# Kernel tuning notes

Hardware: AMD Instinct MI355X
Metric: run time of the kernel (lower is better)

## Reference

```python
import jax, jax.numpy as jnp
import numpy as np

B, S, D_IN, D_OUT, DEPTH = 4, 2048, 2048, 2048, 11
N_NODES = 2 ** (DEPTH + 1) - 1  # 4095


def setup_inputs() -> dict:
    key = jax.random.key(0)
    k1, k2, k3 = jax.random.split(key, 3)
    x = jax.random.normal(k1, (B, S, D_IN), dtype=jnp.float32)
    # scale weights like Linear init (~1/sqrt(fan_in)) to keep logits sane
    w_in = jax.random.normal(k2, (N_NODES, D_IN), dtype=jnp.float32) * (1.0 / np.sqrt(D_IN))
    w_out = jax.random.normal(k3, (D_OUT, N_NODES), dtype=jnp.float32) * (1.0 / np.sqrt(N_NODES))
    return {"x": x, "w_in": w_in, "w_out": w_out}


def reference(x, w_in, w_out):
    # x: [B,S,D_in]; w_in: [n_nodes, D_in]; w_out: [D_out, n_nodes]
    b, s, _ = x.shape
    cur = jnp.zeros((b, s), dtype=jnp.int32)
    nodes, logits = [], []
    for _ in range(DEPTH + 1):  # fixed, small depth loop (12 iters)
        nodes.append(cur)
        coeffs = w_in[cur]                       # [B,S,D_in] data-dependent gather
        score = jnp.einsum('bsd,bsd->bs', x, coeffs)  # per-token dot product
        logits.append(score)
        cur = cur * 2 + (score >= 0).astype(jnp.int32) + 1
    all_nodes = jnp.stack(nodes, axis=-1)        # [B,S,depth+1]
    all_logits = jnp.stack(logits, axis=-1)      # [B,S,depth+1]
    sel = w_out.T[all_nodes]                     # [B,S,depth+1,D_out]
    mlp1 = jax.nn.gelu(all_logits, approximate=False)  # torch nn.GELU default = exact erf
    return jnp.einsum('bsl,bslw->bsw', mlp1, sel)      # [B,S,D_out]
```

## Files before the change

### kernel.cpp

```cpp
#include <hip/hip_runtime.h>


#define D_IN    2048
#define D_OUT   2048
#define DEPTHP1 12
#define N_NODES 4095
#define N_TOK   8192
#define N_LEAF  2048

typedef float f4 __attribute__((ext_vector_type(4)));

__global__ __launch_bounds__(256) void transpose_wout64z(
    const float* __restrict__ in, float* __restrict__ out,
    int* __restrict__ hc ) {
    __shared__ float tile[64][65];
    const int fb = blockIdx.y * 64 + blockIdx.x;
    const int tx = threadIdx.x;
    const int ty = threadIdx.y;
    if (fb < 16) {
        const int i = fb * 256 + ty * 64 + tx;
        hc[i] = 0;
    }
    const int n0 = blockIdx.x * 64;
    const int j0 = blockIdx.y * 64;
    const int n = n0 + tx;
#pragma unroll
    for (int k = 0; k < 16; k++) {
        const int r = ty * 16 + k;
        if (n < N_NODES) tile[r][tx] = in[(size_t)(j0 + r) * N_NODES + n];
    }
    __syncthreads();
#pragma unroll
    for (int k = 0; k < 16; k++) {
        const int r = ty * 16 + k;
        const int nn = n0 + r;
        if (nn < N_NODES) out[(size_t)nn * D_OUT + (j0 + tx)] = tile[tx][r];
    }
}

__global__ __launch_bounds__(256) void phaseA(
    const float* __restrict__ x,
    const float* __restrict__ w_in,
    float* __restrict__ g_all,
    int* __restrict__ leaf,
    int* __restrict__ hist) {
    extern __shared__ float xs[];
    const int wave  = threadIdx.x >> 6;
    const int lane  = threadIdx.x & 63;
    const int token = blockIdx.x * 4 + wave;

    float4* xw = (float4*)(xs) + wave * (D_IN / 4);
    const float4* xrow = (const float4*)(x + (size_t)token * D_IN);
#pragma unroll
    for (int c = 0; c < 8; c++) xw[lane + 64 * c] = xrow[lane + 64 * c];

    int cur = 0;
#pragma unroll
    for (int l = 0; l < DEPTHP1; l++) {
        const float4* wrow = (const float4*)(w_in + (size_t)cur * D_IN);
        float p0 = 0.f, p1 = 0.f, p2 = 0.f, p3 = 0.f;
#pragma unroll
        for (int c = 0; c < 8; c++) {
            const float4 wc = wrow[lane + 64 * c];
            const float4 xc = xw[lane + 64 * c];
            float* p = (c < 2) ? &p0 : (c < 4) ? &p1 : (c < 6) ? &p2 : &p3;
            *p += wc.x * xc.x + wc.y * xc.y + wc.z * xc.z + wc.w * xc.w;
        }
        float part = (p0 + p1) + (p2 + p3);
#pragma unroll
        for (int off = 32; off >= 1; off >>= 1)
            part += __shfl_xor(part, off, 64);
        const float score = part;
        cur = 2 * cur + 1 + (score >= 0.f ? 1 : 0);
        const float g = 0.5f * score * (1.0f + erff(score * 0.70710678118654752f));
        if (lane == 0) g_all[token * DEPTHP1 + l] = g;
    }
    if (lane == 0) {
        const int leafid = ((cur - 1) >> 1) - (N_LEAF - 1);
        leaf[token] = leafid;
        atomicAdd(&hist[leafid], 1);
    }
}

__global__ __launch_bounds__(256) void scatter_scan(
    const int* __restrict__ leaf, const int* __restrict__ hist,
    int* __restrict__ cnt, const float* __restrict__ g_all,
    int* __restrict__ order, float* __restrict__ g_sorted,
    int* __restrict__ lf_sorted) {
    __shared__ int voff[N_LEAF];
    __shared__ int partial[256];
    const int t = threadIdx.x;
    int v[8];
    int sum = 0;
#pragma unroll
    for (int k = 0; k < 8; k++) {
        v[k] = hist[t * 8 + k];
        sum += v[k];
    }
    partial[t] = sum;
    __syncthreads();
    for (int off = 1; off < 256; off <<= 1) {
        const int pv = partial[t];
        const int po = (t >= off) ? partial[t - off] : 0;
        __syncthreads();
        partial[t] = pv + po;
        __syncthreads();
    }
    int base = (t > 0) ? partial[t - 1] : 0;
#pragma unroll
    for (int k = 0; k < 8; k++) {
        voff[t * 8 + k] = base;
        base += v[k];
    }
    __syncthreads();

    const int tok = blockIdx.x * 256 + t;
    const int lf  = leaf[tok];
    const int pos = voff[lf] + atomicAdd(&cnt[lf], 1);
    order[pos] = tok;
    lf_sorted[pos] = lf;
#pragma unroll
    for (int l = 0; l < DEPTHP1; l++)
        g_sorted[(size_t)pos * DEPTHP1 + l] = g_all[(size_t)tok * DEPTHP1 + l];
}

__global__ __launch_bounds__(256) void phaseB_cols(
    const float* __restrict__ w_out_t,
    const float* __restrict__ g_sorted,
    const int* __restrict__ order,
    const int* __restrict__ lf_sorted,
    float* __restrict__ out) {
    const int b   = blockIdx.x;
    const int xcd = b & 7;
    const int j   = b >> 3;
    const int tr  = xcd * 128 + (j >> 1);
    const int ct  = j & 1;
    const int t   = threadIdx.x;
    const size_t coff = (size_t)ct * 1024 + (size_t)t * 4;

    const int start = tr * 8;
    const int end   = start + 8;

    int pos = start;
    while (pos < end) {
        const int lf = lf_sorted[pos];
        const int L  = lf + N_LEAF;
        f4 w[DEPTHP1];
#pragma unroll
        for (int l = 0; l < DEPTHP1; l++) {
            const int node = (L >> (DEPTHP1 - 1 - l)) - 1;
            w[l] = *(const f4*)(w_out_t + (size_t)node * D_OUT + coff);
        }
        do {
            const int tok = order[pos];
            const float* gp = g_sorted + (size_t)pos * DEPTHP1;
            f4 acc = {0.f, 0.f, 0.f, 0.f};
#pragma unroll
            for (int l = 0; l < DEPTHP1; l++)
                acc += gp[l] * w[l];
            __builtin_nontemporal_store(
                acc, (f4*)(out + (size_t)tok * D_OUT + coff));
            pos++;
        } while (pos < end && lf_sorted[pos] == lf);
    }
}

__global__ __launch_bounds__(256) void transpose_wout64(
    const float* __restrict__ in, float* __restrict__ out) {
    __shared__ float tile[64][65];
    const int n0 = blockIdx.x * 64;
    const int j0 = blockIdx.y * 64;
    const int tx = threadIdx.x;
    const int ty = threadIdx.y;
    const int n = n0 + tx;
#pragma unroll
    for (int k = 0; k < 16; k++) {
        const int r = ty * 16 + k;
        if (n < N_NODES) tile[r][tx] = in[(size_t)(j0 + r) * N_NODES + n];
    }
    __syncthreads();
#pragma unroll
    for (int k = 0; k < 16; k++) {
        const int r = ty * 16 + k;
        const int nn = n0 + r;
        if (nn < N_NODES) out[(size_t)nn * D_OUT + (j0 + tx)] = tile[tx][r];
    }
}

template <bool TRANSPOSED>
__global__ __launch_bounds__(256) void fff_fused(
    const float* __restrict__ x, const float* __restrict__ w_in,
    const float* __restrict__ w_out, float* __restrict__ out) {
    const int wave  = threadIdx.x >> 6;
    const int lane  = threadIdx.x & 63;
    const int token = blockIdx.x * 4 + wave;
    const float4* xrow = (const float4*)(x + (size_t)token * D_IN);
    float xf[32];
#pragma unroll
    for (int c = 0; c < 8; c++) {
        float4 xc = xrow[lane + 64 * c];
        xf[c * 4 + 0] = xc.x; xf[c * 4 + 1] = xc.y;
        xf[c * 4 + 2] = xc.z; xf[c * 4 + 3] = xc.w;
    }
    float acc[32];
#pragma unroll
    for (int k = 0; k < 32; k++) acc[k] = 0.f;
    int cur = 0;
#pragma unroll
    for (int l = 0; l < DEPTHP1; l++) {
        const float4* wrow = (const float4*)(w_in + (size_t)cur * D_IN);
        float part = 0.f;
#pragma unroll
        for (int c = 0; c < 8; c++) {
            float4 wc = wrow[lane + 64 * c];
            part += wc.x * xf[c * 4 + 0]; part += wc.y * xf[c * 4 + 1];
            part += wc.z * xf[c * 4 + 2]; part += wc.w * xf[c * 4 + 3];
        }
#pragma unroll
        for (int off = 32; off >= 1; off >>= 1) part += __shfl_xor(part, off, 64);
        const float score = part;
        const float g = 0.5f * score * (1.0f + erff(score * 0.70710678118654752f));
        if (TRANSPOSED) {
            const float4* orow = (const float4*)(w_out + (size_t)cur * D_OUT);
#pragma unroll
            for (int c = 0; c < 8; c++) {
                float4 oc = orow[lane + 64 * c];
                acc[c * 4 + 0] += g * oc.x; acc[c * 4 + 1] += g * oc.y;
                acc[c * 4 + 2] += g * oc.z; acc[c * 4 + 3] += g * oc.w;
            }
        } else {
#pragma unroll
            for (int c = 0; c < 8; c++)
#pragma unroll
                for (int k = 0; k < 4; k++) {
                    const int j = (lane + 64 * c) * 4 + k;
                    acc[c * 4 + k] += g * w_out[(size_t)j * N_NODES + cur];
                }
        }
        cur = 2 * cur + 1 + (score >= 0.f ? 1 : 0);
    }
    float4* outrow = (float4*)(out + (size_t)token * D_OUT);
#pragma unroll
    for (int c = 0; c < 8; c++) {
        float4 o;
        o.x = acc[c * 4 + 0]; o.y = acc[c * 4 + 1];
        o.z = acc[c * 4 + 2]; o.w = acc[c * 4 + 3];
        outrow[lane + 64 * c] = o;
    }
}

extern "C" void kernel_launch(void* const* d_in, const int* in_sizes, int n_in,
                              void* d_out, int out_size, void* d_ws, size_t ws_size,
                              hipStream_t stream) {
    (void)in_sizes; (void)n_in; (void)out_size;
    const float* x     = (const float*)d_in[0];
    const float* w_in  = (const float*)d_in[1];
    const float* w_out = (const float*)d_in[2];
    float* out = (float*)d_out;

    const size_t wt_bytes   = (size_t)N_NODES * D_OUT * sizeof(float);
    const size_t g_bytes    = (size_t)N_TOK * DEPTHP1 * sizeof(float);
    const size_t leaf_bytes = (size_t)N_TOK * sizeof(int);
    const size_t ord_bytes  = (size_t)N_TOK * sizeof(int);
    const size_t hist_bytes = (size_t)N_LEAF * sizeof(int);
    const size_t cnt_bytes  = (size_t)N_LEAF * sizeof(int);
    const size_t gs_bytes   = g_bytes;
    const size_t lfs_bytes  = (size_t)N_TOK * sizeof(int);
    const size_t need = wt_bytes + g_bytes + leaf_bytes + ord_bytes +
                        hist_bytes + cnt_bytes + gs_bytes + lfs_bytes + 64;

    if (ws_size >= need) {
        char* p = (char*)d_ws;
        float* w_out_t  = (float*)p;  p += wt_bytes;
        float* g_all    = (float*)p;  p += g_bytes;
        int*   leaf     = (int*)p;    p += leaf_bytes;
        int*   order    = (int*)p;    p += ord_bytes;
        int*   hist     = (int*)p;    p += hist_bytes;
        int*   cnt      = (int*)p;    p += cnt_bytes;
        float* g_sorted = (float*)p;  p += gs_bytes;
        int*   lf_sorted= (int*)p;

        transpose_wout64z<<<dim3(64, 32), dim3(64, 4), 0, stream>>>(
            w_out, w_out_t, hist);
        phaseA<<<N_TOK / 4, 256, 4 * D_IN * sizeof(float), stream>>>(
            x, w_in, g_all, leaf, hist);
        scatter_scan<<<N_TOK / 256, 256, 0, stream>>>(leaf, hist, cnt, g_all,
                                                      order, g_sorted, lf_sorted);
        phaseB_cols<<<2048, 256, 0, stream>>>(w_out_t, g_sorted, order,
                                              lf_sorted, out);
    } else if (ws_size >= wt_bytes) {
        float* w_out_t = (float*)d_ws;
        transpose_wout64<<<dim3((N_NODES + 63) / 64, D_OUT / 64), dim3(64, 4),
                           0, stream>>>(w_out, w_out_t);
        fff_fused<true><<<N_TOK / 4, 256, 0, stream>>>(x, w_in, w_out_t, out);
    } else {
        fff_fused<false><<<N_TOK / 4, 256, 0, stream>>>(x, w_in, w_out, out);
    }
}
```

Baseline: 224.9 us.

## Fuse four-stage pipeline into one cooperative kernel with grid syncs

Replaces the four separate launches (transpose, tree traversal, scan/scatter, output gather) with a single cooperative kernel of 1024 blocks that uses grid-wide barriers between stages. In the first stage, blocks interleave transpose tiles with traversal work so the memory-heavy transpose overlaps the latency-bound tree walk. The aim is to remove launch gaps and tail effects between kernels. The cost is three grid barriers, and the scan stage occupies only 32 blocks while the rest wait. If the cooperative launch fails, the code falls back to the old multi-kernel path.

```diff
diff --git a/kernel.cpp b/kernel.cpp
--- a/kernel.cpp
+++ b/kernel.cpp
@@ -1,5 +1,8 @@
 #include <hip/hip_runtime.h>
-
+#include <hip/hip_cooperative_groups.h>
+
+
+namespace cg = cooperative_groups;
 
 #define D_IN    2048
 #define D_OUT   2048
@@ -7,12 +10,184 @@
 #define N_NODES 4095
 #define N_TOK   8192
 #define N_LEAF  2048
+#define MEGA_G  1024
 
 typedef float f4 __attribute__((ext_vector_type(4)));
+
+__global__ __launch_bounds__(256) void fff_mega(
+    const float* __restrict__ x,
+    const float* __restrict__ w_in,
+    const float* __restrict__ w_out,
+    float* __restrict__ w_out_t,
+    float* __restrict__ g_all,
+    int* __restrict__ leaf,
+    int* __restrict__ hc,
+    int* __restrict__ order,
+    float* __restrict__ g_sorted,
+    int* __restrict__ lf_sorted,
+    float* __restrict__ out) {
+    extern __shared__ char smem[];
+    cg::grid_group grid = cg::this_grid();
+    const int bid = blockIdx.x;
+    const int tid = threadIdx.x;
+
+    if (tid < 4) hc[bid * 4 + tid] = 0;
+    __threadfence();
+    grid.sync();
+
+    int seq[4];
+    if ((bid & 1) == 0) {
+        seq[0] = 2048 + bid; seq[1] = bid;
+        seq[2] = 3072 + bid; seq[3] = 1024 + bid;
+    } else {
+        seq[0] = bid;        seq[1] = 2048 + bid;
+        seq[2] = 1024 + bid; seq[3] = 3072 + bid;
+    }
+#pragma unroll
+    for (int s = 0; s < 4; s++) {
+        __syncthreads();
+        const int u = seq[s];
+        if (u < 2048) {
+            float (*tile)[65] = (float(*)[65])smem;
+            const int tx = tid & 63;
+            const int ty = tid >> 6;
+            const int n0 = (u & 63) * 64;
+            const int j0 = (u >> 6) * 64;
+            const int n = n0 + tx;
+#pragma unroll
+            for (int k = 0; k < 16; k++) {
+                const int r = ty * 16 + k;
+                if (n < N_NODES)
+                    tile[r][tx] = w_out[(size_t)(j0 + r) * N_NODES + n];
+            }
+            __syncthreads();
+#pragma unroll
+            for (int k = 0; k < 16; k++) {
+                const int r = ty * 16 + k;
+                const int nn = n0 + r;
+                if (nn < N_NODES)
+                    w_out_t[(size_t)nn * D_OUT + (j0 + tx)] = tile[tx][r];
+            }
+        } else {
+            const int q     = u - 2048;
+            const int wave  = tid >> 6;
+            const int lane  = tid & 63;
+            const int token = q * 4 + wave;
+            float4* xw = (float4*)smem + wave * (D_IN / 4);
+            const float4* xrow = (const float4*)(x + (size_t)token * D_IN);
+#pragma unroll
+            for (int c = 0; c < 8; c++) xw[lane + 64 * c] = xrow[lane + 64 * c];
+            int cur = 0;
+#pragma unroll
+            for (int l = 0; l < DEPTHP1; l++) {
+                const float4* wrow = (const float4*)(w_in + (size_t)cur * D_IN);
+                float p0 = 0.f, p1 = 0.f, p2 = 0.f, p3 = 0.f;
+#pragma unroll
+                for (int c = 0; c < 8; c++) {
+                    const float4 wc = wrow[lane + 64 * c];
+                    const float4 xc = xw[lane + 64 * c];
+                    float* p = (c < 2) ? &p0 : (c < 4) ? &p1 : (c < 6) ? &p2 : &p3;
+                    *p += wc.x * xc.x + wc.y * xc.y + wc.z * xc.z + wc.w * xc.w;
+                }
+                float part = (p0 + p1) + (p2 + p3);
+#pragma unroll
+                for (int off = 32; off >= 1; off >>= 1)
+                    part += __shfl_xor(part, off, 64);
+                const float score = part;
+                cur = 2 * cur + 1 + (score >= 0.f ? 1 : 0);
+                const float g =
+                    0.5f * score * (1.0f + erff(score * 0.70710678118654752f));
+                if (lane == 0) g_all[token * DEPTHP1 + l] = g;
+            }
+            if (lane == 0) {
+                const int leafid = ((cur - 1) >> 1) - (N_LEAF - 1);
+                leaf[token] = leafid;
+                atomicAdd(&hc[leafid], 1);
+            }
+        }
+    }
+    __threadfence();
+    grid.sync();
+
+    if (bid < 32) {
+        int* voff    = (int*)smem;
+        int* partial = (int*)smem + N_LEAF;
+        const int* hist = hc;
+        int* cnt = hc + N_LEAF;
+        int v[8];
+        int sum = 0;
+#pragma unroll
+        for (int k = 0; k < 8; k++) {
+            v[k] = hist[tid * 8 + k];
+            sum += v[k];
+        }
+        partial[tid] = sum;
+        __syncthreads();
+        for (int off = 1; off < 256; off <<= 1) {
+            const int pv = partial[tid];
+            const int po = (tid >= off) ? partial[tid - off] : 0;
+            __syncthreads();
+            partial[tid] = pv + po;
+            __syncthreads();
+        }
+        int base = (tid > 0) ? partial[tid - 1] : 0;
+#pragma unroll
+        for (int k = 0; k < 8; k++) {
+            voff[tid * 8 + k] = base;
+            base += v[k];
+        }
+        __syncthreads();
+
+        const int tok = bid * 256 + tid;
+        const int lf  = leaf[tok];
+        const int pos = voff[lf] + atomicAdd(&cnt[lf], 1);
+        order[pos] = tok;
+        lf_sorted[pos] = lf;
+#pragma unroll
+        for (int l = 0; l < DEPTHP1; l++)
+            g_sorted[(size_t)pos * DEPTHP1 + l] =
+                g_all[(size_t)tok * DEPTHP1 + l];
+    }
+    __threadfence();
+    grid.sync();
+
+    for (int u = bid; u < 2048; u += MEGA_G) {
+        const int xcd = u & 7;
+        const int j   = u >> 3;
+        const int tr  = xcd * 128 + (j >> 1);
+        const int ct  = j & 1;
+        const size_t coff = (size_t)ct * 1024 + (size_t)tid * 4;
+
+        const int start = tr * 8;
+        const int end   = start + 8;
+        int pos = start;
+        while (pos < end) {
+            const int lf = lf_sorted[pos];
+            const int L  = lf + N_LEAF;
+            f4 w[DEPTHP1];
+#pragma unroll
+            for (int l = 0; l < DEPTHP1; l++) {
+                const int node = (L >> (DEPTHP1 - 1 - l)) - 1;
+                w[l] = *(const f4*)(w_out_t + (size_t)node * D_OUT + coff);
+            }
+            do {
+                const int tok = order[pos];
+                const float* gp = g_sorted + (size_t)pos * DEPTHP1;
+                f4 acc = {0.f, 0.f, 0.f, 0.f};
+#pragma unroll
+                for (int l = 0; l < DEPTHP1; l++)
+                    acc += gp[l] * w[l];
+                __builtin_nontemporal_store(
+                    acc, (f4*)(out + (size_t)tok * D_OUT + coff));
+                pos++;
+            } while (pos < end && lf_sorted[pos] == lf);
+        }
+    }
+}
 
 __global__ __launch_bounds__(256) void transpose_wout64z(
     const float* __restrict__ in, float* __restrict__ out,
-    int* __restrict__ hc ) {
+    int* __restrict__ hc) {
     __shared__ float tile[64][65];
     const int fb = blockIdx.y * 64 + blockIdx.x;
     const int tx = threadIdx.x;
@@ -39,21 +214,17 @@
 }
 
 __global__ __launch_bounds__(256) void phaseA(
-    const float* __restrict__ x,
-    const float* __restrict__ w_in,
-    float* __restrict__ g_all,
-    int* __restrict__ leaf,
+    const float* __restrict__ x, const float* __restrict__ w_in,
+    float* __restrict__ g_all, int* __restrict__ leaf,
     int* __restrict__ hist) {
     extern __shared__ float xs[];
     const int wave  = threadIdx.x >> 6;
     const int lane  = threadIdx.x & 63;
     const int token = blockIdx.x * 4 + wave;
-
     float4* xw = (float4*)(xs) + wave * (D_IN / 4);
     const float4* xrow = (const float4*)(x + (size_t)token * D_IN);
 #pragma unroll
     for (int c = 0; c < 8; c++) xw[lane + 64 * c] = xrow[lane + 64 * c];
-
     int cur = 0;
 #pragma unroll
     for (int l = 0; l < DEPTHP1; l++) {
@@ -113,7 +284,6 @@
         base += v[k];
     }
     __syncthreads();
-
     const int tok = blockIdx.x * 256 + t;
     const int lf  = leaf[tok];
     const int pos = voff[lf] + atomicAdd(&cnt[lf], 1);
@@ -125,10 +295,8 @@
 }
 
 __global__ __launch_bounds__(256) void phaseB_cols(
-    const float* __restrict__ w_out_t,
-    const float* __restrict__ g_sorted,
-    const int* __restrict__ order,
-    const int* __restrict__ lf_sorted,
+    const float* __restrict__ w_out_t, const float* __restrict__ g_sorted,
+    const int* __restrict__ order, const int* __restrict__ lf_sorted,
     float* __restrict__ out) {
     const int b   = blockIdx.x;
     const int xcd = b & 7;
@@ -137,10 +305,8 @@
     const int ct  = j & 1;
     const int t   = threadIdx.x;
     const size_t coff = (size_t)ct * 1024 + (size_t)t * 4;
-
     const int start = tr * 8;
     const int end   = start + 8;
-
     int pos = start;
     while (pos < end) {
         const int lf = lf_sorted[pos];
@@ -262,12 +428,11 @@
     const size_t g_bytes    = (size_t)N_TOK * DEPTHP1 * sizeof(float);
     const size_t leaf_bytes = (size_t)N_TOK * sizeof(int);
     const size_t ord_bytes  = (size_t)N_TOK * sizeof(int);
-    const size_t hist_bytes = (size_t)N_LEAF * sizeof(int);
-    const size_t cnt_bytes  = (size_t)N_LEAF * sizeof(int);
+    const size_t hc_bytes   = (size_t)(2 * N_LEAF) * sizeof(int);
     const size_t gs_bytes   = g_bytes;
     const size_t lfs_bytes  = (size_t)N_TOK * sizeof(int);
     const size_t need = wt_bytes + g_bytes + leaf_bytes + ord_bytes +
-                        hist_bytes + cnt_bytes + gs_bytes + lfs_bytes + 64;
+                        hc_bytes + gs_bytes + lfs_bytes + 64;
 
     if (ws_size >= need) {
         char* p = (char*)d_ws;
@@ -275,19 +440,27 @@
         float* g_all    = (float*)p;  p += g_bytes;
         int*   leaf     = (int*)p;    p += leaf_bytes;
         int*   order    = (int*)p;    p += ord_bytes;
-        int*   hist     = (int*)p;    p += hist_bytes;
-        int*   cnt      = (int*)p;    p += cnt_bytes;
+        int*   hc       = (int*)p;    p += hc_bytes;
         float* g_sorted = (float*)p;  p += gs_bytes;
         int*   lf_sorted= (int*)p;
 
-        transpose_wout64z<<<dim3(64, 32), dim3(64, 4), 0, stream>>>(
-            w_out, w_out_t, hist);
-        phaseA<<<N_TOK / 4, 256, 4 * D_IN * sizeof(float), stream>>>(
-            x, w_in, g_all, leaf, hist);
-        scatter_scan<<<N_TOK / 256, 256, 0, stream>>>(leaf, hist, cnt, g_all,
-                                                      order, g_sorted, lf_sorted);
-        phaseB_cols<<<2048, 256, 0, stream>>>(w_out_t, g_sorted, order,
-                                              lf_sorted, out);
+        void* args[] = {
+            (void*)&x, (void*)&w_in, (void*)&w_out, (void*)&w_out_t,
+            (void*)&g_all, (void*)&leaf, (void*)&hc, (void*)&order,
+            (void*)&g_sorted, (void*)&lf_sorted, (void*)&out};
+        hipError_t e = hipLaunchCooperativeKernel(
+            (const void*)fff_mega, dim3(MEGA_G), dim3(256), args,
+            32768, stream);
+        if (e != hipSuccess) {
+            transpose_wout64z<<<dim3(64, 32), dim3(64, 4), 0, stream>>>(
+                w_out, w_out_t, hc);
+            phaseA<<<N_TOK / 4, 256, 4 * D_IN * sizeof(float), stream>>>(
+                x, w_in, g_all, leaf, hc);
+            scatter_scan<<<N_TOK / 256, 256, 0, stream>>>(
+                leaf, hc, hc + N_LEAF, g_all, order, g_sorted, lf_sorted);
+            phaseB_cols<<<2048, 256, 0, stream>>>(w_out_t, g_sorted, order,
+                                                  lf_sorted, out);
+        }
     } else if (ws_size >= wt_bytes) {
         float* w_out_t = (float*)d_ws;
         transpose_wout64<<<dim3((N_NODES + 63) / 64, D_OUT / 64), dim3(64, 4),
```

Result: slower. 735.1 us (+226.9%).
